# Kernel tuning notes

Hardware: AMD Instinct MI355X
Metric: run time of the kernel (lower is better)

Reference implementation:

```python
import math
import jax, jax.numpy as jnp
import numpy as np

B, T, E = 2, 2048, 4096
H, HKV = 32, 8
DH = E // H          # 128
G = H // HKV         # 4

ROPE_THETA = 500000.0
ROPE_FACTOR = 32.0
HI_FREQ_FACTOR = 4.0
LO_FREQ_FACTOR = 1.0
ORIG_CTX = 8192


def setup_inputs() -> dict:
    key = jax.random.key(0)
    kx, kq, kk, kv, ko = jax.random.split(key, 5)
    w = lambda k, shape: jax.random.normal(k, shape, jnp.float32) * 0.02
    return {
        "x": jax.random.normal(kx, (B, T, E), jnp.float32),
        # torch nn.Linear stores weight as [out, in]; y = x @ W.T
        "Wq": w(kq, (E, E)),
        "Wk": w(kk, (HKV * DH, E)),
        "Wv": w(kv, (HKV * DH, E)),
        "Wo": w(ko, (E, E)),
    }


def _rope_cos_sin(t_len):
    # faithful port of Llama3MHAttention._rope_cos_sin (llama3 rope scaling)
    inv_freq = 1.0 / (ROPE_THETA ** (jnp.arange(0, DH, 2, dtype=jnp.float32) / DH))
    wavelen = 2.0 * math.pi / inv_freq
    cut_lo = ORIG_CTX / HI_FREQ_FACTOR   # wavelen_cutoff[0]
    cut_hi = ORIG_CTX / LO_FREQ_FACTOR   # wavelen_cutoff[1]
    inv_freq = jnp.where(wavelen > cut_hi, inv_freq / ROPE_FACTOR, inv_freq)
    smooth = (ORIG_CTX / wavelen - LO_FREQ_FACTOR) / (HI_FREQ_FACTOR - LO_FREQ_FACTOR)
    smoothed = (1.0 - smooth) * inv_freq / ROPE_FACTOR + smooth * inv_freq
    # exactly as in the source: ~(wavelen < cutoff[1]) & ~(wavelen > cutoff[0])
    is_medium = (~(wavelen < cut_hi)) & (~(wavelen > cut_lo))
    inv_freq = jnp.where(is_medium, smoothed, inv_freq)
    pos = jnp.arange(t_len, dtype=jnp.float32)          # T_past = 0
    freqs = pos[:, None] * inv_freq[None, :]            # [T, DH/2]
    emb = jnp.concatenate([freqs, freqs], axis=-1)      # [T, DH]
    return jnp.cos(emb), jnp.sin(emb)


def _rotate_half(x):
    x1, x2 = jnp.split(x, 2, axis=-1)
    return jnp.concatenate([-x2, x1], axis=-1)


def reference(x, Wq, Wk, Wv, Wo):
    b, t, _ = x.shape
    q = (x @ Wq.T).reshape(b, t, H, DH).transpose(0, 2, 1, 3)      # [B,H,T,Dh]
    k = (x @ Wk.T).reshape(b, t, HKV, DH).transpose(0, 2, 1, 3)    # [B,Hkv,T,Dh]
    v = (x @ Wv.T).reshape(b, t, HKV, DH).transpose(0, 2, 1, 3)    # [B,Hkv,T,Dh]

    cos, sin = _rope_cos_sin(t)
    cos = cos.astype(x.dtype)[None, None]   # [1,1,T,Dh]
    sin = sin.astype(x.dtype)[None, None]
    q = q * cos + _rotate_half(q) * sin
    k = k * cos + _rotate_half(k) * sin

    qg = q.reshape(b, HKV, G, t, DH)                                # GQA grouping
    scores = jnp.einsum(
        'bhgtd,bhkd->bhgtk', qg.astype(jnp.float32), k.astype(jnp.float32)
    ) / math.sqrt(DH)                                               # [B,Hkv,G,T,T] fp32
    causal = jnp.tril(jnp.ones((t, t), dtype=bool))
    scores = jnp.where(causal[None, None, None], scores,
                       jnp.finfo(jnp.float32).min)
    attn = jax.nn.softmax(scores, axis=-1).astype(x.dtype)
    ctx = jnp.einsum('bhgtk,bhkd->bhgtd', attn, v)                  # [B,Hkv,G,T,Dh]
    out = ctx.reshape(b, H, t, DH).transpose(0, 2, 1, 3).reshape(b, t, E)
    return out @ Wo.T
```

## Files before the change

### kernel.cpp

```cpp
#include <hip/hip_runtime.h>
#include <cstdint>
#include <cstddef>


typedef __bf16 bf16_t;
typedef float  f32x4  __attribute__((ext_vector_type(4)));
typedef __bf16 bf16x8 __attribute__((ext_vector_type(8)));
typedef __bf16 bf16x4 __attribute__((ext_vector_type(4)));

static constexpr int kB   = 2;
static constexpr int kT   = 2048;
static constexpr int kE   = 4096;
static constexpr int kH   = 32;
static constexpr int kHKV = 8;
static constexpr int kDH  = 128;
static constexpr int kNQKV = kE + 2 * kHKV * kDH;
static constexpr int kM    = kB * kT;

__device__ __forceinline__ void gll16(const void* g, void* l) {
  __builtin_amdgcn_global_load_lds(
      (__attribute__((address_space(1))) void*)g,
      (__attribute__((address_space(3))) void*)l, 16, 0, 0);
}

__global__ void cast_f32_bf16_k(const float* __restrict__ in,
                                bf16_t* __restrict__ out, int n4) {
  int i = blockIdx.x * 256 + threadIdx.x;
  if (i >= n4) return;
  float4 v = reinterpret_cast<const float4*>(in)[i];
  bf16x4 o;
  o[0] = (__bf16)v.x; o[1] = (__bf16)v.y; o[2] = (__bf16)v.z; o[3] = (__bf16)v.w;
  reinterpret_cast<bf16x4*>(out)[i] = o;
}

__global__ void rope_table_k(float* __restrict__ cosT, float* __restrict__ sinT) {
  int idx = blockIdx.x * 256 + threadIdx.x;
  if (idx >= kT * 64) return;
  int t = idx >> 6, i = idx & 63;
  float ex  = (float)i / 64.0f;
  float inv = powf(500000.0f, -ex);
  float wl  = 6.283185307179586f / inv;
  const float cut_lo = 8192.0f / 4.0f;
  const float cut_hi = 8192.0f / 1.0f;
  float inv2 = (wl > cut_hi) ? inv * (1.0f / 32.0f) : inv;
  float smooth   = (8192.0f / wl - 1.0f) * (1.0f / 3.0f);
  float smoothed = (1.0f - smooth) * inv2 * (1.0f / 32.0f) + smooth * inv2;
  bool  medium   = (!(wl < cut_hi)) && (!(wl > cut_lo));
  float invf = medium ? smoothed : inv2;
  float f = (float)t * invf;
  cosT[idx] = cosf(f);
  sinT[idx] = sinf(f);
}

__global__ void rope_q_k(const bf16_t* __restrict__ QKV,
                         const float* __restrict__ cosT,
                         const float* __restrict__ sinT,
                         bf16_t* __restrict__ Qr) {
  int idx = blockIdx.x * 256 + threadIdx.x;
  if (idx >= kB * kT * kH * 64) return;
  int i = idx & 63;
  int h = (idx >> 6) & 31;
  int t = (idx >> 11) & 2047;
  int b = idx >> 22;
  const bf16_t* src = QKV + (size_t)(b * kT + t) * kNQKV + h * kDH + i;
  float q1 = (float)src[0], q2 = (float)src[64];
  float c = cosT[(t << 6) + i], s = sinT[(t << 6) + i];
  const float sc = 0.08838834764831845f;
  bf16_t* dst = Qr + ((size_t)(b * kH + h) * kT + t) * kDH + i;
  dst[0]  = (__bf16)((q1 * c - q2 * s) * sc);
  dst[64] = (__bf16)((q2 * c + q1 * s) * sc);
}

__global__ void rope_k_k(const bf16_t* __restrict__ QKV,
                         const float* __restrict__ cosT,
                         const float* __restrict__ sinT,
                         bf16_t* __restrict__ Kr) {
  int idx = blockIdx.x * 256 + threadIdx.x;
  if (idx >= kB * kT * kHKV * 64) return;
  int i = idx & 63;
  int h = (idx >> 6) & 7;
  int t = (idx >> 9) & 2047;
  int b = idx >> 20;
  const bf16_t* src = QKV + (size_t)(b * kT + t) * kNQKV + kE + h * kDH + i;
  float k1 = (float)src[0], k2 = (float)src[64];
  float c = cosT[(t << 6) + i], s = sinT[(t << 6) + i];
  bf16_t* dst = Kr + ((size_t)(b * kHKV + h) * kT + t) * kDH + i;
  dst[0]  = (__bf16)(k1 * c - k2 * s);
  dst[64] = (__bf16)(k2 * c + k1 * s);
}

__global__ void vtrans_k(const bf16_t* __restrict__ QKV, bf16_t* __restrict__ Vt) {
  __shared__ bf16_t tile[64 * 130];
  int bidx = blockIdx.x;
  int tt = bidx & 31;
  int h  = (bidx >> 5) & 7;
  int b  = bidx >> 8;
  int tid = threadIdx.x;
  int t0 = tt * 64;
  for (int it = 0; it < 32; ++it) {
    int e = it * 256 + tid;
    int tr = e >> 7, d = e & 127;
    tile[tr * 130 + d] =
        QKV[(size_t)(b * kT + t0 + tr) * kNQKV + kE + kHKV * kDH + h * kDH + d];
  }
  __syncthreads();
  for (int j = 0; j < 32; ++j) {
    int o = j * 256 + tid;
    int d = o >> 6, tr = o & 63;
    Vt[((size_t)(b * kHKV + h) * kDH + d) * kT + t0 + tr] = tile[tr * 130 + d];
  }
}

template <bool OUT_BF16>
__global__ __launch_bounds__(256, 2)
void gemm_nt_k(const bf16_t* __restrict__ A, const bf16_t* __restrict__ Bm,
               void* __restrict__ Cv, int M, int N, int K) {
  __shared__ bf16_t As[128 * 32];
  __shared__ bf16_t Bs[128 * 32];
  const int tid = threadIdx.x;
  const int lane = tid & 63, wid = tid >> 6;
  const int l16 = lane & 15, lg = lane >> 4;
  const int row0 = blockIdx.x * 128, col0 = blockIdx.y * 128;
  const int wr = wid >> 1, wc = wid & 1;

  const int s_row = wid * 16 + (lane >> 2);
  const int s_col = (lane & 3) * 8;
  const bf16_t* Ag = A  + (size_t)(row0 + s_row) * K + s_col;
  const bf16_t* Bg = Bm + (size_t)(col0 + s_row) * K + s_col;
  char* AsB = (char*)As + wid * 1024;
  char* BsB = (char*)Bs + wid * 1024;

  const int aoff0 = (wr * 64 + l16) * 32 + lg * 8;
  const int boff0 = (wc * 64 + l16) * 32 + lg * 8;

  f32x4 acc[4][4] = {};
  for (int kt = 0; kt < K; kt += 32) {
    gll16(Ag + kt,                 AsB);
    gll16(Ag + kt + (size_t)64 * K, AsB + 4096);
    gll16(Bg + kt,                 BsB);
    gll16(Bg + kt + (size_t)64 * K, BsB + 4096);
    __syncthreads();
    bf16x8 af[4], bfr[4];
#pragma unroll
    for (int m = 0; m < 4; ++m)
      af[m] = *reinterpret_cast<const bf16x8*>(&As[aoff0 + m * 512]);
#pragma unroll
    for (int n = 0; n < 4; ++n)
      bfr[n] = *reinterpret_cast<const bf16x8*>(&Bs[boff0 + n * 512]);
#pragma unroll
    for (int m = 0; m < 4; ++m)
#pragma unroll
      for (int n = 0; n < 4; ++n)
        acc[m][n] = __builtin_amdgcn_mfma_f32_16x16x32_bf16(af[m], bfr[n],
                                                            acc[m][n], 0, 0, 0);
    __syncthreads();
  }

  const int crow = row0 + wr * 64 + lg * 4;
  const int ccol = col0 + wc * 64 + l16;
#pragma unroll
  for (int m = 0; m < 4; ++m)
#pragma unroll
    for (int n = 0; n < 4; ++n)
#pragma unroll
      for (int j = 0; j < 4; ++j) {
        size_t idx = (size_t)(crow + m * 16 + j) * N + (ccol + n * 16);
        if constexpr (OUT_BF16)
          ((bf16_t*)Cv)[idx] = (__bf16)acc[m][n][j];
        else
          ((float*)Cv)[idx] = acc[m][n][j];
      }
}

__global__ __launch_bounds__(256, 2)
void flash_k(const bf16_t* __restrict__ Qr, const bf16_t* __restrict__ Kr,
             const bf16_t* __restrict__ Vt, bf16_t* __restrict__ Ctx) {
  __shared__ bf16_t Ks[64 * 128];
  __shared__ bf16_t Vs[128 * 64];
  __shared__ bf16_t Ps[4][16][72];

  const int bid = blockIdx.x;
  const int qt = bid & 31;
  const int h  = (bid >> 5) & 31;
  const int b  = bid >> 10;
  const int hkv = h >> 2;
  const int tid = threadIdx.x, lane = tid & 63, w = tid >> 6;
  const int l16 = lane & 15, lg = lane >> 4;

  const bf16_t* Qg = Qr +
      ((size_t)(b * kH + h) * kT + qt * 64 + w * 16 + l16) * kDH + lg * 8;
  bf16x8 qf[4];
#pragma unroll
  for (int kk = 0; kk < 4; ++kk)
    qf[kk] = *reinterpret_cast<const bf16x8*>(Qg + kk * 32);

  const bf16_t* Kg = Kr + (size_t)(b * kHKV + hkv) * kT * kDH;
  const bf16_t* Vg = Vt + (size_t)(b * kHKV + hkv) * kDH * kT;

  const int k_srow = w * 4 + lg;
  const int k_scolb = l16 * 16;
  const int v_srow = w * 8 + (lane >> 3);
  const int v_scolb = (lane & 7) * 16;
  char* KsB = (char*)Ks + w * 1024;
  char* VsB = (char*)Vs + w * 1024;

  float m_run[4] = {-1e30f, -1e30f, -1e30f, -1e30f};
  float l_run[4] = {0.f, 0.f, 0.f, 0.f};
  f32x4 acc_o[8] = {};

  const int nkv = qt + 1;
  for (int it = 0; it < nkv; ++it) {
    const int kv0 = it * 64;
#pragma unroll
    for (int r = 0; r < 4; ++r) {
      int krow = r * 16 + k_srow;
      int kcb  = k_scolb ^ ((krow & 7) << 4);
      gll16(Kg + (size_t)(kv0 + krow) * kDH + (kcb >> 1), KsB + r * 4096);
      int vrow = r * 32 + v_srow;
      int vcb  = v_scolb ^ ((vrow & 7) << 4);
      gll16(Vg + (size_t)vrow * kT + kv0 + (vcb >> 1), VsB + r * 4096);
    }
    __syncthreads();

    f32x4 sc[4] = {};
#pragma unroll
    for (int kk = 0; kk < 4; ++kk) {
#pragma unroll
      for (int nf = 0; nf < 4; ++nf) {
        int row = nf * 16 + l16;
        int cb  = (kk * 64 + lg * 16) ^ ((row & 7) << 4);
        bf16x8 kf = *reinterpret_cast<const bf16x8*>((const char*)Ks + row * 256 + cb);
        sc[nf] = __builtin_amdgcn_mfma_f32_16x16x32_bf16(qf[kk], kf, sc[nf], 0, 0, 0);
      }
    }
    if (it == qt) {
#pragma unroll
      for (int nf = 0; nf < 4; ++nf) {
        int key = kv0 + nf * 16 + l16;
#pragma unroll
        for (int j = 0; j < 4; ++j) {
          int qrow = qt * 64 + w * 16 + lg * 4 + j;
          if (key > qrow) sc[nf][j] = -1e30f;
        }
      }
    }
#pragma unroll
    for (int j = 0; j < 4; ++j) {
      float mx = fmaxf(fmaxf(sc[0][j], sc[1][j]), fmaxf(sc[2][j], sc[3][j]));
      mx = fmaxf(mx, __shfl_xor(mx, 1));
      mx = fmaxf(mx, __shfl_xor(mx, 2));
      mx = fmaxf(mx, __shfl_xor(mx, 4));
      mx = fmaxf(mx, __shfl_xor(mx, 8));
      float mnew = fmaxf(m_run[j], mx);
      float alpha = __expf(m_run[j] - mnew);
      m_run[j] = mnew;
      float ssum = 0.f;
#pragma unroll
      for (int nf = 0; nf < 4; ++nf) {
        float p = __expf(sc[nf][j] - mnew);
        sc[nf][j] = p;
        ssum += p;
      }
      ssum += __shfl_xor(ssum, 1);
      ssum += __shfl_xor(ssum, 2);
      ssum += __shfl_xor(ssum, 4);
      ssum += __shfl_xor(ssum, 8);
      l_run[j] = l_run[j] * alpha + ssum;
#pragma unroll
      for (int nf = 0; nf < 8; ++nf) acc_o[nf][j] *= alpha;
    }
#pragma unroll
    for (int nf = 0; nf < 4; ++nf)
#pragma unroll
      for (int j = 0; j < 4; ++j)
        Ps[w][lg * 4 + j][nf * 16 + l16] = (__bf16)sc[nf][j];
    __syncthreads();
#pragma unroll
    for (int kk2 = 0; kk2 < 2; ++kk2) {
      bf16x8 pf = *reinterpret_cast<const bf16x8*>(&Ps[w][l16][kk2 * 32 + lg * 8]);
#pragma unroll
      for (int nf = 0; nf < 8; ++nf) {
        int d = nf * 16 + l16;
        int cb = (kk2 * 64 + lg * 16) ^ ((d & 7) << 4);
        bf16x8 vf = *reinterpret_cast<const bf16x8*>((const char*)Vs + d * 128 + cb);
        acc_o[nf] = __builtin_amdgcn_mfma_f32_16x16x32_bf16(pf, vf, acc_o[nf], 0, 0, 0);
      }
    }
    __syncthreads();
  }

  const int tglob = qt * 64 + w * 16 + lg * 4;
#pragma unroll
  for (int j = 0; j < 4; ++j) {
    float inv_l = 1.0f / l_run[j];
#pragma unroll
    for (int nf = 0; nf < 8; ++nf)
      Ctx[((size_t)(b * kT + tglob + j) * kH + h) * kDH + nf * 16 + l16] =
          (__bf16)(acc_o[nf][j] * inv_l);
  }
}

extern "C" void kernel_launch(void* const* d_in, const int* in_sizes, int n_in,
                              void* d_out, int out_size, void* d_ws, size_t ws_size,
                              hipStream_t stream) {
  (void)in_sizes; (void)n_in; (void)out_size; (void)ws_size;
  const float* x  = (const float*)d_in[0];
  const float* Wq = (const float*)d_in[1];
  const float* Wk = (const float*)d_in[2];
  const float* Wv = (const float*)d_in[3];
  const float* Wo = (const float*)d_in[4];
  float* out = (float*)d_out;

  char* ws = (char*)d_ws;
  size_t off = 0;
  auto alloc = [&](size_t bytes) -> char* {
    char* p = ws + off;
    off += (bytes + 255) & ~(size_t)255;
    return p;
  };
  bf16_t* xb    = (bf16_t*)alloc((size_t)kM * kE * 2);
  bf16_t* Wqkvb = (bf16_t*)alloc((size_t)kNQKV * kE * 2);
  bf16_t* Wob   = (bf16_t*)alloc((size_t)kE * kE * 2);
  bf16_t* QKV   = (bf16_t*)alloc((size_t)kM * kNQKV * 2);
  float*  cosT  = (float*)alloc((size_t)kT * 64 * 4);
  float*  sinT  = (float*)alloc((size_t)kT * 64 * 4);
  bf16_t* Qr  = Wqkvb;
  bf16_t* Kr  = Wqkvb + (size_t)kE * kE;
  bf16_t* Vt  = Wqkvb + (size_t)(kE + kHKV * kDH) * kE;
  bf16_t* Ctx = xb;

  cast_f32_bf16_k<<<16384, 256, 0, stream>>>(x, xb, kM * kE / 4);
  cast_f32_bf16_k<<<16384, 256, 0, stream>>>(Wq, Wqkvb, kE * kE / 4);
  cast_f32_bf16_k<<<4096, 256, 0, stream>>>(Wk, Wqkvb + (size_t)kE * kE,
                                            kHKV * kDH * kE / 4);
  cast_f32_bf16_k<<<4096, 256, 0, stream>>>(Wv, Wqkvb + (size_t)(kE + kHKV * kDH) * kE,
                                            kHKV * kDH * kE / 4);
  cast_f32_bf16_k<<<16384, 256, 0, stream>>>(Wo, Wob, kE * kE / 4);
  rope_table_k<<<512, 256, 0, stream>>>(cosT, sinT);

  {
    dim3 g(kM / 128, kNQKV / 128);
    gemm_nt_k<true><<<g, 256, 0, stream>>>(xb, Wqkvb, QKV, kM, kNQKV, kE);
  }
  rope_q_k<<<32768, 256, 0, stream>>>(QKV, cosT, sinT, Qr);
  rope_k_k<<<8192, 256, 0, stream>>>(QKV, cosT, sinT, Kr);
  vtrans_k<<<512, 256, 0, stream>>>(QKV, Vt);
  flash_k<<<kB * kH * (kT / 64), 256, 0, stream>>>(Qr, Kr, Vt, Ctx);
  {
    dim3 g(kM / 128, kE / 128);
    gemm_nt_k<false><<<g, 256, 0, stream>>>(Ctx, Wob, out, kM, kE, kE);
  }
}
```

Baseline: 939.6 us.

## Double-buffer K/V tiles, widen flash query tile, reorder blocks longest-first

Each flash-attention block now handles 128 queries (two 16-row MFMA tiles per wave), so every K/V fragment read from LDS feeds two MFMAs. K/V loads for the next tile are issued into a second LDS buffer while the current tile is being computed, and a single barrier per iteration replaces the three used before. Block IDs are remapped so the longest causal tiles start first and consecutive blocks are spread across XCDs, and the P staging buffer gains an XOR swizzle. The cost is more LDS (about 80KB per block) and more registers, which may lower occupancy below the two blocks per CU that the launch bounds request.

```diff
diff --git a/kernel.cpp b/kernel.cpp
--- a/kernel.cpp
+++ b/kernel.cpp
@@ -175,24 +175,28 @@
 __global__ __launch_bounds__(256, 2)
 void flash_k(const bf16_t* __restrict__ Qr, const bf16_t* __restrict__ Kr,
              const bf16_t* __restrict__ Vt, bf16_t* __restrict__ Ctx) {
-  __shared__ bf16_t Ks[64 * 128];
-  __shared__ bf16_t Vs[128 * 64];
-  __shared__ bf16_t Ps[4][16][72];
-
-  const int bid = blockIdx.x;
-  const int qt = bid & 31;
-  const int h  = (bid >> 5) & 31;
-  const int b  = bid >> 10;
+  __shared__ bf16_t Ks[2][64 * 128];
+  __shared__ bf16_t Vs[2][128 * 64];
+  __shared__ bf16_t Ps[4][32 * 64];
+
+  const int gid  = blockIdx.x;
+  const int wgid = (gid & 7) * 128 + (gid >> 3);
+  const int qt = 15 - (wgid & 15);
+  const int h  = (wgid >> 4) & 31;
+  const int b  = wgid >> 9;
   const int hkv = h >> 2;
   const int tid = threadIdx.x, lane = tid & 63, w = tid >> 6;
   const int l16 = lane & 15, lg = lane >> 4;
+  const int qbase = qt * 128;
 
   const bf16_t* Qg = Qr +
-      ((size_t)(b * kH + h) * kT + qt * 64 + w * 16 + l16) * kDH + lg * 8;
-  bf16x8 qf[4];
-#pragma unroll
-  for (int kk = 0; kk < 4; ++kk)
-    qf[kk] = *reinterpret_cast<const bf16x8*>(Qg + kk * 32);
+      ((size_t)(b * kH + h) * kT + qbase + w * 32 + l16) * kDH + lg * 8;
+  bf16x8 qf[2][4];
+#pragma unroll
+  for (int m = 0; m < 2; ++m)
+#pragma unroll
+    for (int kk = 0; kk < 4; ++kk)
+      qf[m][kk] = *reinterpret_cast<const bf16x8*>(Qg + m * 16 * kDH + kk * 32);
 
   const bf16_t* Kg = Kr + (size_t)(b * kHKV + hkv) * kT * kDH;
   const bf16_t* Vg = Vt + (size_t)(b * kHKV + hkv) * kDH * kT;
@@ -201,102 +205,152 @@
   const int k_scolb = l16 * 16;
   const int v_srow = w * 8 + (lane >> 3);
   const int v_scolb = (lane & 7) * 16;
-  char* KsB = (char*)Ks + w * 1024;
-  char* VsB = (char*)Vs + w * 1024;
-
-  float m_run[4] = {-1e30f, -1e30f, -1e30f, -1e30f};
-  float l_run[4] = {0.f, 0.f, 0.f, 0.f};
-  f32x4 acc_o[8] = {};
-
-  const int nkv = qt + 1;
+
+  float m_run[2][4], l_run[2][4];
+#pragma unroll
+  for (int m = 0; m < 2; ++m)
+#pragma unroll
+    for (int j = 0; j < 4; ++j) { m_run[m][j] = -1e30f; l_run[m][j] = 0.f; }
+  f32x4 acc_o[2][8] = {};
+
+  const int nkv = 2 * qt + 2;
+
+#pragma unroll
+  for (int r = 0; r < 4; ++r) {
+    int krow = r * 16 + k_srow;
+    int kcb  = k_scolb ^ ((krow & 7) << 4);
+    gll16(Kg + (size_t)krow * kDH + (kcb >> 1),
+          (char*)Ks[0] + w * 1024 + r * 4096);
+    int vrow = r * 32 + v_srow;
+    int vcb  = v_scolb ^ ((vrow & 7) << 4);
+    gll16(Vg + (size_t)vrow * kT + (vcb >> 1),
+          (char*)Vs[0] + w * 1024 + r * 4096);
+  }
+
   for (int it = 0; it < nkv; ++it) {
+    const int cur = it & 1;
     const int kv0 = it * 64;
-#pragma unroll
-    for (int r = 0; r < 4; ++r) {
-      int krow = r * 16 + k_srow;
-      int kcb  = k_scolb ^ ((krow & 7) << 4);
-      gll16(Kg + (size_t)(kv0 + krow) * kDH + (kcb >> 1), KsB + r * 4096);
-      int vrow = r * 32 + v_srow;
-      int vcb  = v_scolb ^ ((vrow & 7) << 4);
-      gll16(Vg + (size_t)vrow * kT + kv0 + (vcb >> 1), VsB + r * 4096);
+    asm volatile("s_waitcnt vmcnt(0)" ::: "memory");
+    __builtin_amdgcn_s_barrier();
+    __builtin_amdgcn_sched_barrier(0);
+    if (it + 1 < nkv) {
+      const int kv1 = kv0 + 64;
+#pragma unroll
+      for (int r = 0; r < 4; ++r) {
+        int krow = r * 16 + k_srow;
+        int kcb  = k_scolb ^ ((krow & 7) << 4);
+        gll16(Kg + (size_t)(kv1 + krow) * kDH + (kcb >> 1),
+              (char*)Ks[cur ^ 1] + w * 1024 + r * 4096);
+        int vrow = r * 32 + v_srow;
+        int vcb  = v_scolb ^ ((vrow & 7) << 4);
+        gll16(Vg + (size_t)vrow * kT + kv1 + (vcb >> 1),
+              (char*)Vs[cur ^ 1] + w * 1024 + r * 4096);
+      }
     }
-    __syncthreads();
-
-    f32x4 sc[4] = {};
+
+    f32x4 sc[2][4] = {};
 #pragma unroll
     for (int kk = 0; kk < 4; ++kk) {
 #pragma unroll
       for (int nf = 0; nf < 4; ++nf) {
         int row = nf * 16 + l16;
         int cb  = (kk * 64 + lg * 16) ^ ((row & 7) << 4);
-        bf16x8 kf = *reinterpret_cast<const bf16x8*>((const char*)Ks + row * 256 + cb);
-        sc[nf] = __builtin_amdgcn_mfma_f32_16x16x32_bf16(qf[kk], kf, sc[nf], 0, 0, 0);
+        bf16x8 kf = *reinterpret_cast<const bf16x8*>(
+            (const char*)Ks[cur] + row * 256 + cb);
+#pragma unroll
+        for (int m = 0; m < 2; ++m)
+          sc[m][nf] = __builtin_amdgcn_mfma_f32_16x16x32_bf16(
+              qf[m][kk], kf, sc[m][nf], 0, 0, 0);
       }
     }
-    if (it == qt) {
+    if (it >= nkv - 2) {
 #pragma unroll
       for (int nf = 0; nf < 4; ++nf) {
         int key = kv0 + nf * 16 + l16;
 #pragma unroll
-        for (int j = 0; j < 4; ++j) {
-          int qrow = qt * 64 + w * 16 + lg * 4 + j;
-          if (key > qrow) sc[nf][j] = -1e30f;
+        for (int m = 0; m < 2; ++m)
+#pragma unroll
+          for (int j = 0; j < 4; ++j) {
+            int qrow = qbase + w * 32 + m * 16 + lg * 4 + j;
+            if (key > qrow) sc[m][nf][j] = -1e30f;
+          }
+      }
+    }
+#pragma unroll
+    for (int m = 0; m < 2; ++m)
+#pragma unroll
+      for (int j = 0; j < 4; ++j) {
+        float mx = fmaxf(fmaxf(sc[m][0][j], sc[m][1][j]),
+                         fmaxf(sc[m][2][j], sc[m][3][j]));
+        mx = fmaxf(mx, __shfl_xor(mx, 1));
+        mx = fmaxf(mx, __shfl_xor(mx, 2));
+        mx = fmaxf(mx, __shfl_xor(mx, 4));
+        mx = fmaxf(mx, __shfl_xor(mx, 8));
+        float mnew = fmaxf(m_run[m][j], mx);
+        float alpha = __expf(m_run[m][j] - mnew);
+        m_run[m][j] = mnew;
+        float ssum = 0.f;
+#pragma unroll
+        for (int nf = 0; nf < 4; ++nf) {
+          float p = __expf(sc[m][nf][j] - mnew);
+          sc[m][nf][j] = p;
+          ssum += p;
         }
-      }
-    }
-#pragma unroll
-    for (int j = 0; j < 4; ++j) {
-      float mx = fmaxf(fmaxf(sc[0][j], sc[1][j]), fmaxf(sc[2][j], sc[3][j]));
-      mx = fmaxf(mx, __shfl_xor(mx, 1));
-      mx = fmaxf(mx, __shfl_xor(mx, 2));
-      mx = fmaxf(mx, __shfl_xor(mx, 4));
-      mx = fmaxf(mx, __shfl_xor(mx, 8));
-      float mnew = fmaxf(m_run[j], mx);
-      float alpha = __expf(m_run[j] - mnew);
-      m_run[j] = mnew;
-      float ssum = 0.f;
-#pragma unroll
-      for (int nf = 0; nf < 4; ++nf) {
-        float p = __expf(sc[nf][j] - mnew);
-        sc[nf][j] = p;
-        ssum += p;
-      }
-      ssum += __shfl_xor(ssum, 1);
-      ssum += __shfl_xor(ssum, 2);
-      ssum += __shfl_xor(ssum, 4);
-      ssum += __shfl_xor(ssum, 8);
-      l_run[j] = l_run[j] * alpha + ssum;
-#pragma unroll
-      for (int nf = 0; nf < 8; ++nf) acc_o[nf][j] *= alpha;
-    }
-#pragma unroll
-    for (int nf = 0; nf < 4; ++nf)
-#pragma unroll
-      for (int j = 0; j < 4; ++j)
-        Ps[w][lg * 4 + j][nf * 16 + l16] = (__bf16)sc[nf][j];
-    __syncthreads();
+        ssum += __shfl_xor(ssum, 1);
+        ssum += __shfl_xor(ssum, 2);
+        ssum += __shfl_xor(ssum, 4);
+        ssum += __shfl_xor(ssum, 8);
+        l_run[m][j] = l_run[m][j] * alpha + ssum;
+#pragma unroll
+        for (int nf = 0; nf < 8; ++nf) acc_o[m][nf][j] *= alpha;
+      }
+#pragma unroll
+    for (int m = 0; m < 2; ++m)
+#pragma unroll
+      for (int j = 0; j < 4; ++j) {
+        int prow = m * 16 + lg * 4 + j;
+        int swz  = (prow & 7) << 4;
+#pragma unroll
+        for (int nf = 0; nf < 4; ++nf) {
+          int wbyte = ((nf * 16 + l16) * 2) ^ swz;
+          *(bf16_t*)((char*)Ps[w] + prow * 128 + wbyte) = (__bf16)sc[m][nf][j];
+        }
+      }
 #pragma unroll
     for (int kk2 = 0; kk2 < 2; ++kk2) {
-      bf16x8 pf = *reinterpret_cast<const bf16x8*>(&Ps[w][l16][kk2 * 32 + lg * 8]);
+      bf16x8 pf[2];
+#pragma unroll
+      for (int m = 0; m < 2; ++m) {
+        int prow = m * 16 + l16;
+        int cb = (kk2 * 64 + lg * 16) ^ ((prow & 7) << 4);
+        pf[m] = *reinterpret_cast<const bf16x8*>(
+            (const char*)Ps[w] + prow * 128 + cb);
+      }
 #pragma unroll
       for (int nf = 0; nf < 8; ++nf) {
         int d = nf * 16 + l16;
         int cb = (kk2 * 64 + lg * 16) ^ ((d & 7) << 4);
-        bf16x8 vf = *reinterpret_cast<const bf16x8*>((const char*)Vs + d * 128 + cb);
-        acc_o[nf] = __builtin_amdgcn_mfma_f32_16x16x32_bf16(pf, vf, acc_o[nf], 0, 0, 0);
+        bf16x8 vf = *reinterpret_cast<const bf16x8*>(
+            (const char*)Vs[cur] + d * 128 + cb);
+#pragma unroll
+        for (int m = 0; m < 2; ++m)
+          acc_o[m][nf] = __builtin_amdgcn_mfma_f32_16x16x32_bf16(
+              pf[m], vf, acc_o[m][nf], 0, 0, 0);
       }
     }
-    __syncthreads();
-  }
-
-  const int tglob = qt * 64 + w * 16 + lg * 4;
-#pragma unroll
-  for (int j = 0; j < 4; ++j) {
-    float inv_l = 1.0f / l_run[j];
-#pragma unroll
-    for (int nf = 0; nf < 8; ++nf)
-      Ctx[((size_t)(b * kT + tglob + j) * kH + h) * kDH + nf * 16 + l16] =
-          (__bf16)(acc_o[nf][j] * inv_l);
+  }
+
+#pragma unroll
+  for (int m = 0; m < 2; ++m) {
+    const int tglob = qbase + w * 32 + m * 16 + lg * 4;
+#pragma unroll
+    for (int j = 0; j < 4; ++j) {
+      float inv_l = 1.0f / l_run[m][j];
+#pragma unroll
+      for (int nf = 0; nf < 8; ++nf)
+        Ctx[((size_t)(b * kT + tglob + j) * kH + h) * kDH + nf * 16 + l16] =
+            (__bf16)(acc_o[m][nf][j] * inv_l);
+    }
   }
 }
 
@@ -345,7 +399,7 @@
   rope_q_k<<<32768, 256, 0, stream>>>(QKV, cosT, sinT, Qr);
   rope_k_k<<<8192, 256, 0, stream>>>(QKV, cosT, sinT, Kr);
   vtrans_k<<<512, 256, 0, stream>>>(QKV, Vt);
-  flash_k<<<kB * kH * (kT / 64), 256, 0, stream>>>(Qr, Kr, Vt, Ctx);
+  flash_k<<<kB * kH * (kT / 128), 256, 0, stream>>>(Qr, Kr, Vt, Ctx);
   {
     dim3 g(kM / 128, kE / 128);
     gemm_nt_k<false><<<g, 256, 0, stream>>>(Ctx, Wob, out, kM, kE, kE);
```

Measured after the change: 854.8 us. -9.0%, faster.
